# Optimization experiments

Measured on AMD Instinct MI355X. Metric: run time of the kernel, lower is better.

The kernel has to match this reference:

```python
import jax, jax.numpy as jnp
import numpy as np

N_NODES = 100000
N_EDGES = 1600000


def setup_inputs() -> dict:
    key = jax.random.key(0)
    ks = jax.random.split(key, 6)
    x = jax.random.normal(ks[0], (N_NODES, 166), dtype=jnp.float32)
    edge_index = jax.random.randint(ks[1], (2, N_EDGES), 0, N_NODES, dtype=jnp.int64)
    s = 0.05
    return {
        "x": x,
        "edge_index": edge_index,
        "W1l": jax.random.normal(ks[2], (166, 128), dtype=jnp.float32) * s,
        "b1": jnp.zeros((128,), dtype=jnp.float32),
        "W1r": jax.random.normal(ks[3], (166, 128), dtype=jnp.float32) * s,
        "W2l": jax.random.normal(ks[4], (128, 2), dtype=jnp.float32) * s,
        "b2": jnp.zeros((2,), dtype=jnp.float32),
        "W2r": jax.random.normal(ks[5], (128, 2), dtype=jnp.float32) * s,
    }


def _sage_mean_agg(h, src, dst, n_nodes):
    # mean over incoming edges (PyG SAGEConv default aggr='mean');
    # nodes with no in-edges get zeros.
    summed = jax.ops.segment_sum(h[src], dst, num_segments=n_nodes)
    deg = jax.ops.segment_sum(jnp.ones_like(dst, dtype=h.dtype), dst,
                              num_segments=n_nodes)
    return summed / jnp.maximum(deg, 1.0)[:, None]


def reference(x, edge_index, W1l, b1, W1r, W2l, b2, W2r):
    src, dst = edge_index[0], edge_index[1]
    n = x.shape[0]
    # layer 1: out = lin_l(mean_agg(x)) + lin_r(x)
    agg1 = _sage_mean_agg(x, src, dst, n)
    h = agg1 @ W1l + b1 + x @ W1r
    h = jax.nn.relu(h)
    # dropout p=0.5 is identity in eval mode
    # layer 2
    agg2 = _sage_mean_agg(h, src, dst, n)
    out = agg2 @ W2l + b2 + h @ W2r
    return jax.nn.log_softmax(out, axis=1)
```

## Files before the change

### kernel.cpp

```cpp
#include <hip/hip_runtime.h>
#include <hip/hip_bf16.h>
#include <math.h>

#define N_NODES 100000
#define N_EDGES 1600000
#define FDIM 166
#define HDIM 128
#define KP 192
#define CAP 64
#define YTP 264
#define NXCD 8
#define NODES_PER (N_NODES / NXCD)
#define MBLK 64
#define XCHUNKS 42
#define XPITCH 672
#define TOTCH (MBLK * XCHUNKS)

typedef __attribute__((ext_vector_type(8))) short bf16x8;
typedef __attribute__((ext_vector_type(4))) float f32x4;

#define GLOAD_LDS16(g, l) __builtin_amdgcn_global_load_lds( \
    (const __attribute__((address_space(1))) unsigned int*)(g), \
    (__attribute__((address_space(3))) unsigned int*)(l), 16, 0, 0)

__device__ inline float bf2f(unsigned short s) {
    unsigned int u = ((unsigned int)s) << 16;
    float f; __builtin_memcpy(&f, &u, 4); return f;
}
__device__ inline float bflo(unsigned int u) {
    unsigned int v = u << 16;
    float f; __builtin_memcpy(&f, &v, 4); return f;
}
__device__ inline float bfhi(unsigned int u) {
    unsigned int v = u & 0xffff0000u;
    float f; __builtin_memcpy(&f, &v, 4); return f;
}
__device__ inline unsigned short f2bf(float f) {
    unsigned int u; __builtin_memcpy(&u, &f, 4);
    unsigned int r = u + 0x7fffu + ((u >> 16) & 1u);
    return (unsigned short)(r >> 16);
}
__device__ inline bf16x8 pack8(float4 a, float4 b) {
    union { bf16x8 v; __hip_bfloat162 h[4]; } u;
    u.h[0] = __float22bfloat162_rn(make_float2(a.x, a.y));
    u.h[1] = __float22bfloat162_rn(make_float2(a.z, a.w));
    u.h[2] = __float22bfloat162_rn(make_float2(b.x, b.y));
    u.h[3] = __float22bfloat162_rn(make_float2(b.z, b.w));
    return u.v;
}

__global__ __launch_bounds__(256) void k_fill(const int* __restrict__ ei,
                                              int* __restrict__ cnt,
                                              int* __restrict__ adj) {
    int xcd = blockIdx.x & (NXCD - 1);
    int grp = blockIdx.x >> 3;
    int lo = xcd * NODES_PER, hi = lo + NODES_PER;
    int stride = (gridDim.x >> 3) * 256;
    for (int e = grp * 256 + threadIdx.x; e < N_EDGES; e += stride) {
        int d = __builtin_nontemporal_load(&ei[N_EDGES + e]);
        if (d >= lo && d < hi) {
            int s = __builtin_nontemporal_load(&ei[e]);
            int slot = atomicAdd(&cnt[d], 1);
            if (slot < CAP) adj[d * CAP + slot] = s;
        }
    }
}

__global__ void k_prepw(const float* __restrict__ W1l, const float* __restrict__ W1r,
                        unsigned short* __restrict__ wt) {
    int idx = blockIdx.x * 256 + threadIdx.x;
    int c = idx / KP, k = idx - c * KP;
    float v = 0.f;
    if (k < FDIM)
        v = (c < HDIM) ? W1l[k * HDIM + c] : W1r[k * HDIM + (c - HDIM)];
    wt[idx] = f2bf(v);
}

__global__ __launch_bounds__(256) void k_gemm(
        const float* __restrict__ x, const unsigned short* __restrict__ wt,
        unsigned short* __restrict__ yl, unsigned short* __restrict__ yr) {
    __shared__ __align__(16) char sm[43264];
    int tid = threadIdx.x;
    int r0 = blockIdx.x * MBLK;
    int w = tid >> 6, lane = tid & 63;

    if (tid < 32) *(float*)(sm + TOTCH * 16 + tid * 4) = 0.f;

    {
        int wbase = w * 64;
        #pragma unroll
        for (int rd = 0; rd < 11; ++rd) {
            int base = rd * 256 + wbase;
            if (base < TOTCH) {
                int idx = base + lane;
                int row = idx / XCHUNKS, c = idx - row * XCHUNKS;
                int gr = r0 + row; if (gr > N_NODES - 1) gr = N_NODES - 1;
                const char* src = (const char*)x + (size_t)gr * (FDIM * 4) + c * 16;
                GLOAD_LDS16(src, sm + base * 16);
            }
        }
    }
    __syncthreads();

    int rbase = (w >> 1) * 32;
    int c0 = (w & 1) * 128;
    int l15 = lane & 15, g = lane >> 4;

    f32x4 acc[2][8];
    #pragma unroll
    for (int a = 0; a < 2; a++)
        #pragma unroll
        for (int b = 0; b < 8; b++) acc[a][b] = (f32x4){0.f, 0.f, 0.f, 0.f};

    const char* wb = (const char*)wt;
    int wlane = (c0 + l15) * (KP * 2) + 16 * g;
    int brow0 = (rbase + l15) * XPITCH + 32 * g;
    int brow1 = brow0 + 16 * XPITCH;

    bf16x8 ww[2][8];
    #pragma unroll
    for (int cf = 0; cf < 8; cf++)
        ww[0][cf] = *(const bf16x8*)(wb + wlane + cf * (16 * KP * 2));

    #pragma unroll
    for (int kk = 0; kk < 6; ++kk) {
        int cur = kk & 1, nxt = cur ^ 1;
        if (kk < 5) {
            #pragma unroll
            for (int cf = 0; cf < 8; cf++)
                ww[nxt][cf] = *(const bf16x8*)(wb + wlane + cf * (16 * KP * 2) + (kk + 1) * 64);
        }
        float4 p0 = *(const float4*)(sm + brow0 + kk * 128);
        float4 q0 = *(const float4*)(sm + brow0 + kk * 128 + 16);
        float4 p1 = *(const float4*)(sm + brow1 + kk * 128);
        float4 q1 = *(const float4*)(sm + brow1 + kk * 128 + 16);
        bf16x8 xb0 = pack8(p0, q0);
        bf16x8 xb1 = pack8(p1, q1);
        #pragma unroll
        for (int cf = 0; cf < 8; cf++) {
            acc[0][cf] = __builtin_amdgcn_mfma_f32_16x16x32_bf16(ww[cur][cf], xb0, acc[0][cf], 0, 0, 0);
            acc[1][cf] = __builtin_amdgcn_mfma_f32_16x16x32_bf16(ww[cur][cf], xb1, acc[1][cf], 0, 0, 0);
        }
    }
    __syncthreads();

    #pragma unroll
    for (int rf = 0; rf < 2; rf++) {
        int row = rbase + 16 * rf + l15;
        #pragma unroll
        for (int cf = 0; cf < 8; cf++) {
            int col = c0 + 16 * cf + 4 * g;
            ushort4 o;
            o.x = f2bf(acc[rf][cf][0]); o.y = f2bf(acc[rf][cf][1]);
            o.z = f2bf(acc[rf][cf][2]); o.w = f2bf(acc[rf][cf][3]);
            *(ushort4*)(sm + row * (YTP * 2) + col * 2) = o;
        }
    }
    __syncthreads();

    for (int it = 0; it < 8; ++it) {
        int n = tid + it * 256;
        int row = n >> 5, c16 = n & 31;
        uint4 v = *(const uint4*)(sm + row * (YTP * 2) + c16 * 16);
        int gr = r0 + row;
        if (gr < N_NODES) {
            unsigned short* dst = (c16 < 16) ? yl : yr;
            *(uint4*)((char*)dst + (size_t)gr * 256 + (size_t)(c16 & 15) * 16) = v;
        }
    }
}

__global__ __launch_bounds__(256) void k_agg1(
        const unsigned short* __restrict__ yl, const unsigned short* __restrict__ yr,
        const int* __restrict__ cnt, const int* __restrict__ adj,
        const float* __restrict__ b1,
        const float* __restrict__ W2l, const float* __restrict__ W2r,
        float* __restrict__ zw) {
    int w = threadIdx.x >> 6, lane = threadIdx.x & 63;
    int i = blockIdx.x * 4 + w;
    if (i >= N_NODES) return;
    int deg = cnt[i];
    int n = min(deg, CAP);
    int aidx = adj[i * CAP + lane];
    int half = lane >> 5, fl = lane & 31;
    float A0 = 0.f, A1 = 0.f, A2 = 0.f, A3 = 0.f;
    float B0 = 0.f, B1 = 0.f, B2 = 0.f, B3 = 0.f;
    float C0 = 0.f, C1 = 0.f, C2 = 0.f, C3 = 0.f;
    float D0 = 0.f, D1 = 0.f, D2 = 0.f, D3 = 0.f;
    int j = 0;
    for (; j + 8 <= n; j += 8) {
        int sA = __shfl(aidx, j + half, 64);
        int sB = __shfl(aidx, j + 2 + half, 64);
        int sC = __shfl(aidx, j + 4 + half, 64);
        int sD = __shfl(aidx, j + 6 + half, 64);
        uint2 uA = *(const uint2*)&yl[(size_t)sA * HDIM + 4 * fl];
        uint2 uB = *(const uint2*)&yl[(size_t)sB * HDIM + 4 * fl];
        uint2 uC = *(const uint2*)&yl[(size_t)sC * HDIM + 4 * fl];
        uint2 uD = *(const uint2*)&yl[(size_t)sD * HDIM + 4 * fl];
        A0 += bflo(uA.x); A1 += bfhi(uA.x); A2 += bflo(uA.y); A3 += bfhi(uA.y);
        B0 += bflo(uB.x); B1 += bfhi(uB.x); B2 += bflo(uB.y); B3 += bfhi(uB.y);
        C0 += bflo(uC.x); C1 += bfhi(uC.x); C2 += bflo(uC.y); C3 += bfhi(uC.y);
        D0 += bflo(uD.x); D1 += bfhi(uD.x); D2 += bflo(uD.y); D3 += bfhi(uD.y);
    }
    for (; j < n; j += 2) {
        int je = j + half;
        if (je < n) {
            int s = __shfl(aidx, je, 64);
            uint2 u = *(const uint2*)&yl[(size_t)s * HDIM + 4 * fl];
            A0 += bflo(u.x); A1 += bfhi(u.x); A2 += bflo(u.y); A3 += bfhi(u.y);
        }
    }
    float a0 = A0 + B0 + C0 + D0;
    float a1 = A1 + B1 + C1 + D1;
    float a2 = A2 + B2 + C2 + D2;
    float a3 = A3 + B3 + C3 + D3;
    a0 += __shfl_xor(a0, 32, 64); a1 += __shfl_xor(a1, 32, 64);
    a2 += __shfl_xor(a2, 32, 64); a3 += __shfl_xor(a3, 32, 64);
    float inv = 1.f / (float)max(deg, 1);
    uint2 ur = *(const uint2*)&yr[(size_t)i * HDIM + 4 * fl];
    float4 bb = *(const float4*)&b1[4 * fl];
    float h0 = fmaxf(a0 * inv + bflo(ur.x) + bb.x, 0.f);
    float h1 = fmaxf(a1 * inv + bfhi(ur.x) + bb.y, 0.f);
    float h2 = fmaxf(a2 * inv + bflo(ur.y) + bb.z, 0.f);
    float h3 = fmaxf(a3 * inv + bfhi(ur.y) + bb.w, 0.f);
    float4 wlA = *(const float4*)&W2l[8 * fl];
    float4 wlB = *(const float4*)&W2l[8 * fl + 4];
    float4 wrA = *(const float4*)&W2r[8 * fl];
    float4 wrB = *(const float4*)&W2r[8 * fl + 4];
    float z0 = h0 * wlA.x + h1 * wlA.z + h2 * wlB.x + h3 * wlB.z;
    float z1 = h0 * wlA.y + h1 * wlA.w + h2 * wlB.y + h3 * wlB.w;
    float w0 = h0 * wrA.x + h1 * wrA.z + h2 * wrB.x + h3 * wrB.z;
    float w1 = h0 * wrA.y + h1 * wrA.w + h2 * wrB.y + h3 * wrB.w;
    #pragma unroll
    for (int m = 16; m; m >>= 1) {
        z0 += __shfl_xor(z0, m, 64); z1 += __shfl_xor(z1, m, 64);
        w0 += __shfl_xor(w0, m, 64); w1 += __shfl_xor(w1, m, 64);
    }
    if (lane == 0) {
        float4 o = {z0, z1, w0, w1};
        *(float4*)&zw[i * 4] = o;
    }
}

__global__ void k_out(const float* __restrict__ zw, const int* __restrict__ cnt,
                      const int* __restrict__ adj, const float* __restrict__ b2,
                      float* __restrict__ out) {
    int i = blockIdx.x * 256 + threadIdx.x;
    if (i >= N_NODES) return;
    int deg = cnt[i];
    int n = min(deg, CAP);
    float s0 = 0.f, s1 = 0.f;
    const int* arow = adj + i * CAP;
    for (int j = 0; j < n; j++) {
        int s = arow[j];
        float2 zz = *(const float2*)&zw[s * 4];
        s0 += zz.x; s1 += zz.y;
    }
    float inv = 1.f / (float)max(deg, 1);
    float p0 = s0 * inv + b2[0] + zw[i * 4 + 2];
    float p1 = s1 * inv + b2[1] + zw[i * 4 + 3];
    float mx = fmaxf(p0, p1);
    float lse = mx + logf(expf(p0 - mx) + expf(p1 - mx));
    out[i * 2 + 0] = p0 - lse;
    out[i * 2 + 1] = p1 - lse;
}

extern "C" void kernel_launch(void* const* d_in, const int* in_sizes, int n_in,
                              void* d_out, int out_size, void* d_ws, size_t ws_size,
                              hipStream_t stream) {
    const float* x   = (const float*)d_in[0];
    const int*   ei  = (const int*)d_in[1];
    const float* W1l = (const float*)d_in[2];
    const float* b1  = (const float*)d_in[3];
    const float* W1r = (const float*)d_in[4];
    const float* W2l = (const float*)d_in[5];
    const float* b2  = (const float*)d_in[6];
    const float* W2r = (const float*)d_in[7];
    float* out = (float*)d_out;

    char* ws = (char*)d_ws;
    size_t off = 0;
    auto alloc = [&](size_t bytes) {
        off = (off + 255) & ~(size_t)255;
        void* p = ws + off;
        off += bytes;
        return p;
    };
    int* cnt            = (int*)alloc((size_t)N_NODES * 4);
    int* adj            = (int*)alloc((size_t)N_NODES * CAP * 4);
    unsigned short* wt  = (unsigned short*)alloc((size_t)256 * KP * 2);
    unsigned short* yl  = (unsigned short*)alloc((size_t)N_NODES * HDIM * 2);
    unsigned short* yr  = (unsigned short*)alloc((size_t)N_NODES * HDIM * 2);
    float* zw           = (float*)alloc((size_t)N_NODES * 4 * 4);
    (void)ws_size; (void)in_sizes; (void)n_in; (void)out_size;

    hipMemsetAsync(cnt, 0, (size_t)N_NODES * 4, stream);
    k_fill<<<2048, 256, 0, stream>>>(ei, cnt, adj);
    k_prepw<<<(256 * KP) / 256, 256, 0, stream>>>(W1l, W1r, wt);
    k_gemm<<<(N_NODES + MBLK - 1) / MBLK, 256, 0, stream>>>(x, wt, yl, yr);
    k_agg1<<<(N_NODES + 3) / 4, 256, 0, stream>>>(yl, yr, cnt, adj, b1, W2l, W2r, zw);
    k_out<<<(N_NODES + 255) / 256, 256, 0, stream>>>(zw, cnt, adj, b2, out);
}
```

Measured before the change: 225.9 us.

## Halve GEMM row tile, fuse memset with weight prep, drop nontemporal loads

The GEMM block now covers 32 rows instead of 64. That halves shared memory and accumulator registers per block and doubles the grid, which should raise occupancy. The weight double-buffer prefetch is removed, so weight loads are no longer overlapped with MFMA, and each block reloads the full weight matrix for half as many rows. The hipMemsetAsync of the degree counters is merged into the weight-prep kernel, saving a launch. Edge-index loads in k_fill switch from nontemporal to normal loads.

```diff
diff --git a/kernel.cpp b/kernel.cpp
--- a/kernel.cpp
+++ b/kernel.cpp
@@ -9,12 +9,12 @@
 #define KP 192
 #define CAP 64
 #define YTP 264
-#define NXCD 8
-#define NODES_PER (N_NODES / NXCD)
-#define MBLK 64
+#define MBLK 32
 #define XCHUNKS 42
 #define XPITCH 672
 #define TOTCH (MBLK * XCHUNKS)
+#define NXCD 8
+#define NODES_PER (N_NODES / NXCD)
 
 typedef __attribute__((ext_vector_type(8))) short bf16x8;
 typedef __attribute__((ext_vector_type(4))) float f32x4;
@@ -47,6 +47,21 @@
     u.h[2] = __float22bfloat162_rn(make_float2(b.x, b.y));
     u.h[3] = __float22bfloat162_rn(make_float2(b.z, b.w));
     return u.v;
+}
+
+__global__ void k_pre(const float* __restrict__ W1l, const float* __restrict__ W1r,
+                      unsigned short* __restrict__ wt, int* __restrict__ cnt) {
+    int idx = blockIdx.x * 256 + threadIdx.x;
+    if (blockIdx.x < 192) {
+        int c = idx / KP, k = idx - c * KP;
+        float v = 0.f;
+        if (k < FDIM)
+            v = (c < HDIM) ? W1l[k * HDIM + c] : W1r[k * HDIM + (c - HDIM)];
+        wt[idx] = f2bf(v);
+    } else {
+        int i = idx - 192 * 256;
+        if (i < N_NODES) cnt[i] = 0;
+    }
 }
 
 __global__ __launch_bounds__(256) void k_fill(const int* __restrict__ ei,
@@ -57,29 +72,19 @@
     int lo = xcd * NODES_PER, hi = lo + NODES_PER;
     int stride = (gridDim.x >> 3) * 256;
     for (int e = grp * 256 + threadIdx.x; e < N_EDGES; e += stride) {
-        int d = __builtin_nontemporal_load(&ei[N_EDGES + e]);
+        int d = ei[N_EDGES + e];
         if (d >= lo && d < hi) {
-            int s = __builtin_nontemporal_load(&ei[e]);
+            int s = ei[e];
             int slot = atomicAdd(&cnt[d], 1);
             if (slot < CAP) adj[d * CAP + slot] = s;
         }
     }
-}
-
-__global__ void k_prepw(const float* __restrict__ W1l, const float* __restrict__ W1r,
-                        unsigned short* __restrict__ wt) {
-    int idx = blockIdx.x * 256 + threadIdx.x;
-    int c = idx / KP, k = idx - c * KP;
-    float v = 0.f;
-    if (k < FDIM)
-        v = (c < HDIM) ? W1l[k * HDIM + c] : W1r[k * HDIM + (c - HDIM)];
-    wt[idx] = f2bf(v);
 }
 
 __global__ __launch_bounds__(256) void k_gemm(
         const float* __restrict__ x, const unsigned short* __restrict__ wt,
         unsigned short* __restrict__ yl, unsigned short* __restrict__ yr) {
-    __shared__ __align__(16) char sm[43264];
+    __shared__ __align__(16) char sm[21760];
     int tid = threadIdx.x;
     int r0 = blockIdx.x * MBLK;
     int w = tid >> 6, lane = tid & 63;
@@ -89,7 +94,7 @@
     {
         int wbase = w * 64;
         #pragma unroll
-        for (int rd = 0; rd < 11; ++rd) {
+        for (int rd = 0; rd < 6; ++rd) {
             int base = rd * 256 + wbase;
             if (base < TOTCH) {
                 int idx = base + lane;
@@ -102,63 +107,47 @@
     }
     __syncthreads();
 
-    int rbase = (w >> 1) * 32;
+    int rbase = (w >> 1) * 16;
     int c0 = (w & 1) * 128;
     int l15 = lane & 15, g = lane >> 4;
 
-    f32x4 acc[2][8];
+    f32x4 acc[8];
     #pragma unroll
-    for (int a = 0; a < 2; a++)
-        #pragma unroll
-        for (int b = 0; b < 8; b++) acc[a][b] = (f32x4){0.f, 0.f, 0.f, 0.f};
+    for (int b = 0; b < 8; b++) acc[b] = (f32x4){0.f, 0.f, 0.f, 0.f};
 
     const char* wb = (const char*)wt;
     int wlane = (c0 + l15) * (KP * 2) + 16 * g;
-    int brow0 = (rbase + l15) * XPITCH + 32 * g;
-    int brow1 = brow0 + 16 * XPITCH;
-
-    bf16x8 ww[2][8];
-    #pragma unroll
-    for (int cf = 0; cf < 8; cf++)
-        ww[0][cf] = *(const bf16x8*)(wb + wlane + cf * (16 * KP * 2));
+    int brow = (rbase + l15) * XPITCH + 32 * g;
 
     #pragma unroll
     for (int kk = 0; kk < 6; ++kk) {
-        int cur = kk & 1, nxt = cur ^ 1;
-        if (kk < 5) {
-            #pragma unroll
-            for (int cf = 0; cf < 8; cf++)
-                ww[nxt][cf] = *(const bf16x8*)(wb + wlane + cf * (16 * KP * 2) + (kk + 1) * 64);
-        }
-        float4 p0 = *(const float4*)(sm + brow0 + kk * 128);
-        float4 q0 = *(const float4*)(sm + brow0 + kk * 128 + 16);
-        float4 p1 = *(const float4*)(sm + brow1 + kk * 128);
-        float4 q1 = *(const float4*)(sm + brow1 + kk * 128 + 16);
-        bf16x8 xb0 = pack8(p0, q0);
-        bf16x8 xb1 = pack8(p1, q1);
-        #pragma unroll
-        for (int cf = 0; cf < 8; cf++) {
-            acc[0][cf] = __builtin_amdgcn_mfma_f32_16x16x32_bf16(ww[cur][cf], xb0, acc[0][cf], 0, 0, 0);
-            acc[1][cf] = __builtin_amdgcn_mfma_f32_16x16x32_bf16(ww[cur][cf], xb1, acc[1][cf], 0, 0, 0);
-        }
+        bf16x8 ww[8];
+        #pragma unroll
+        for (int cf = 0; cf < 8; cf++)
+            ww[cf] = *(const bf16x8*)(wb + wlane + cf * (16 * KP * 2) + kk * 64);
+        float4 p = *(const float4*)(sm + brow + kk * 128);
+        float4 q = *(const float4*)(sm + brow + kk * 128 + 16);
+        bf16x8 xb = pack8(p, q);
+        #pragma unroll
+        for (int cf = 0; cf < 8; cf++)
+            acc[cf] = __builtin_amdgcn_mfma_f32_16x16x32_bf16(ww[cf], xb, acc[cf], 0, 0, 0);
     }
     __syncthreads();
 
-    #pragma unroll
-    for (int rf = 0; rf < 2; rf++) {
-        int row = rbase + 16 * rf + l15;
+    {
+        int row = rbase + l15;
         #pragma unroll
         for (int cf = 0; cf < 8; cf++) {
             int col = c0 + 16 * cf + 4 * g;
             ushort4 o;
-            o.x = f2bf(acc[rf][cf][0]); o.y = f2bf(acc[rf][cf][1]);
-            o.z = f2bf(acc[rf][cf][2]); o.w = f2bf(acc[rf][cf][3]);
+            o.x = f2bf(acc[cf][0]); o.y = f2bf(acc[cf][1]);
+            o.z = f2bf(acc[cf][2]); o.w = f2bf(acc[cf][3]);
             *(ushort4*)(sm + row * (YTP * 2) + col * 2) = o;
         }
     }
     __syncthreads();
 
-    for (int it = 0; it < 8; ++it) {
+    for (int it = 0; it < 4; ++it) {
         int n = tid + it * 256;
         int row = n >> 5, c16 = n & 31;
         uint4 v = *(const uint4*)(sm + row * (YTP * 2) + c16 * 16);
@@ -294,9 +283,8 @@
     float* zw           = (float*)alloc((size_t)N_NODES * 4 * 4);
     (void)ws_size; (void)in_sizes; (void)n_in; (void)out_size;
 
-    hipMemsetAsync(cnt, 0, (size_t)N_NODES * 4, stream);
+    k_pre<<<192 + (N_NODES + 255) / 256, 256, 0, stream>>>(W1l, W1r, wt, cnt);
     k_fill<<<2048, 256, 0, stream>>>(ei, cnt, adj);
-    k_prepw<<<(256 * KP) / 256, 256, 0, stream>>>(W1l, W1r, wt);
     k_gemm<<<(N_NODES + MBLK - 1) / MBLK, 256, 0, stream>>>(x, wt, yl, yr);
     k_agg1<<<(N_NODES + 3) / 4, 256, 0, stream>>>(yl, yr, cnt, adj, b1, W2l, W2r, zw);
     k_out<<<(N_NODES + 255) / 256, 256, 0, stream>>>(zw, cnt, adj, b2, out);
```

Result: slower. 241.8 us (+7.1%).
